# Kernel optimization log

Measured on AMD Instinct MI355X. Metric: run time of the kernel, lower is better.

## Reference

```python
import jax, jax.numpy as jnp
import numpy as np

B, CIN, COUT, T, S = 4, 32, 64, 8, 3   # batch, in-ch, out-ch, num_taps, stencil edge
D, H, W = 32, 64, 64                    # input volume
PAD = 1                                 # zero padding (stride 1) -> same spatial output


def setup_inputs() -> dict:
    key = jax.random.key(0)
    k1, k2, k3, k4 = jax.random.split(key, 4)
    x = jax.random.normal(k1, (B, CIN, D, H, W), jnp.float32)
    stencils = jax.random.normal(k2, (B, T, S, S, S), jnp.float32)
    weight = jax.random.normal(k3, (COUT, CIN, T), jnp.float32) * 0.05
    bias = jax.random.normal(k4, (COUT,), jnp.float32) * 0.05
    return {"x": x, "stencils": stencils, "weight": weight, "bias": bias}


def reference(x, stencils, weight, bias):
    # x: (B,Cin,D,H,W); stencils: (B,T,sx,sy,sz); weight: (Cout,Cin,T); bias: (Cout,)
    b, cin = x.shape[:2]
    t = stencils.shape[1]
    sx, sy, sz = stencils.shape[2:]
    # zero-pad spatially
    xp = jnp.pad(x, ((0, 0), (0, 0), (PAD, PAD), (PAD, PAD), (PAD, PAD)))
    # fold batch into channels -> grouped conv with groups = B*Cin (per-sample stencils)
    x_exp = xp.reshape(1, b * cin, xp.shape[2], xp.shape[3], xp.shape[4])
    # per-sample stencils shared across Cin, one output feature per (b, cin, tap)
    w = jnp.broadcast_to(stencils[:, None], (b, cin, t, sx, sy, sz))
    w = w.reshape(b * cin * t, 1, sx, sy, sz)
    tap = jax.lax.conv_general_dilated(
        x_exp, w,
        window_strides=(1, 1, 1), padding='VALID',
        dimension_numbers=('NCDHW', 'OIDHW', 'NCDHW'),
        feature_group_count=b * cin,
    )  # (1, B*Cin*T, Do, Ho, Wo)
    do, ho, wo = tap.shape[-3:]
    tap = tap.reshape(b, cin, t, do, ho, wo)
    # channel/tap mixing: (B,Cin,T,D,H,W) x (Cout,Cin,T) -> (B,Cout,D,H,W)
    y = jnp.einsum('bctdhw,oct->bodhw', tap, weight)
    return y + bias[None, :, None, None, None]
```

## Files before the change

kernel.cpp:

```cpp
#include <hip/hip_runtime.h>

typedef short bf16x8 __attribute__((ext_vector_type(8)));
typedef float f32x16 __attribute__((ext_vector_type(16)));

typedef const __attribute__((address_space(1))) unsigned int GUint;
typedef __attribute__((address_space(3))) unsigned int LUint;

#define XT_BYTES 37914624ull

__device__ __forceinline__ unsigned short f2bf(float f) {
    unsigned u = __float_as_uint(f);
    return (unsigned short)((u + 0x7FFFu + ((u >> 16) & 1u)) >> 16);
}

__global__ __launch_bounds__(256) void prep_x(const float* __restrict__ x,
                                              uint4* __restrict__ xt) {
    int yp = blockIdx.x;
    int zp = blockIdx.y;
    int b  = blockIdx.z;
    int t  = threadIdx.x;
    size_t rowbase = ((((size_t)b * 34 + zp) * 66 + yp) * 66) * 4;
    bool in_zy = (zp >= 1 && zp <= 32 && yp >= 1 && yp <= 64);
    for (int idx = t; idx < 264; idx += 256) {
        int q, xp;
        if (idx < 256) { q = idx >> 6; xp = idx & 63; }
        else { int k = idx - 256; q = k >> 1; xp = 64 + (k & 1); }
        uint4 v = make_uint4(0u, 0u, 0u, 0u);
        if (in_zy && xp >= 1 && xp <= 64) {
            int d = zp - 1, h = yp - 1, w = xp - 1;
            const float* xb = x + ((((size_t)b * 32 + q * 8) * 32 + d) * 64 + h) * 64 + w;
            unsigned short us[8];
            #pragma unroll
            for (int j = 0; j < 8; ++j)
                us[j] = f2bf(xb[(size_t)j * 131072]);
            v.x = us[0] | ((unsigned)us[1] << 16);
            v.y = us[2] | ((unsigned)us[3] << 16);
            v.z = us[4] | ((unsigned)us[5] << 16);
            v.w = us[6] | ((unsigned)us[7] << 16);
        }
        int pos = q ^ ((xp >> 1) & 3);
        xt[rowbase + (size_t)xp * 4 + pos] = v;
    }
}

__global__ __launch_bounds__(256) void prep_keff(const float* __restrict__ stencils,
                                                 const float* __restrict__ weight,
                                                 uint4* __restrict__ keffg) {
    int i = blockIdx.x * 256 + threadIdx.x;
    if (i >= 4 * 27 * 64 * 4) return;
    int q = i & 3;
    int o = (i >> 2) & 63;
    int br = i >> 8;
    int r = br % 27, b = br / 27;
    float st[8];
    #pragma unroll
    for (int t = 0; t < 8; ++t) st[t] = stencils[((size_t)b * 8 + t) * 27 + r];
    unsigned short us[8];
    #pragma unroll
    for (int j = 0; j < 8; ++j) {
        const float* wp = weight + ((size_t)o * 32 + q * 8 + j) * 8;
        float acc = 0.f;
        #pragma unroll
        for (int t = 0; t < 8; ++t) acc += wp[t] * st[t];
        us[j] = f2bf(acc);
    }
    uint4 v;
    v.x = us[0] | ((unsigned)us[1] << 16);
    v.y = us[2] | ((unsigned)us[3] << 16);
    v.z = us[4] | ((unsigned)us[5] << 16);
    v.w = us[6] | ((unsigned)us[7] << 16);
    int pos = q ^ ((o >> 1) & 3);
    keffg[(((size_t)br * 64 + o) << 2) + pos] = v;
}

#define KBUF 52224

__global__ __launch_bounds__(256, 2) void conv_mfma(
    const uint4* __restrict__ xt, const uint4* __restrict__ keffg,
    const float* __restrict__ bias, float* __restrict__ out) {
    __shared__ __align__(1024) char smem[60416];

    int n = blockIdx.x;
    int xcd = n & 7, local = n >> 3;
    int dt = local & 15;
    int cmb = (local >> 4) | (xcd << 4);
    int ht = cmb & 15, wt = (cmb >> 4) & 1, b = cmb >> 5;

    int tid = threadIdx.x;
    int lane = tid & 63, wid = tid >> 6;
    int nlo = lane & 31, kh = lane >> 5;

    const char* xtc = (const char*)xt;
    const char* kfc = (const char*)keffg;

    for (int row = wid; row < 24; row += 4) {
        int z = row / 6, yy = row - z * 6;
        size_t gbase = ((((size_t)b * 34 + dt * 2 + z) * 66 + ht * 4 + yy) * 66 + wt * 32) * 64;
        int ldsbase = row * 2176;
        #pragma unroll
        for (int cb = 0; cb < 136; cb += 64) {
            int rem = 136 - cb;
            if (lane < rem) {
                __builtin_amdgcn_global_load_lds(
                    (GUint*)(xtc + gbase + (size_t)(cb + lane) * 16),
                    (LUint*)(smem + ldsbase + cb * 16), 16, 0, 0);
            }
        }
    }
    __builtin_amdgcn_global_load_lds(
        (GUint*)(kfc + (size_t)(b * 27) * 4096 + (size_t)(wid * 64 + lane) * 16),
        (LUint*)(smem + KBUF + wid * 1024), 16, 0, 0);
    __syncthreads();

    int z = wid >> 1;
    int ys = (wid & 1) << 1;

    int Badr[2][3];
    #pragma unroll
    for (int s = 0; s < 2; ++s)
        #pragma unroll
        for (int k3 = 0; k3 < 3; ++k3) {
            int xl = nlo + k3;
            int pos = (s * 2 + kh) ^ ((xl >> 1) & 3);
            Badr[s][k3] = (z * 6 + ys) * 2176 + xl * 64 + (pos << 4);
        }
    int Aadr[2];
    #pragma unroll
    for (int s = 0; s < 2; ++s)
        Aadr[s] = nlo * 64 + (((s * 2 + kh) ^ ((nlo >> 1) & 3)) << 4);

    f32x16 acc[2][2];
    #pragma unroll
    for (int mt = 0; mt < 2; ++mt)
        #pragma unroll
        for (int nt = 0; nt < 2; ++nt)
            #pragma unroll
            for (int e = 0; e < 16; ++e) acc[mt][nt][e] = 0.f;

    #pragma unroll
    for (int r = 0; r < 27; ++r) {
        int i3 = r / 9, j3 = (r / 3) % 3, k3 = r % 3;
        if (r < 26) {
            __builtin_amdgcn_global_load_lds(
                (GUint*)(kfc + (size_t)(b * 27 + r + 1) * 4096 + (size_t)(wid * 64 + lane) * 16),
                (LUint*)(smem + KBUF + (((r + 1) & 1) << 12) + wid * 1024), 16, 0, 0);
        }
        int kbase = KBUF + ((r & 1) << 12);
        #pragma unroll
        for (int s = 0; s < 2; ++s) {
            bf16x8 a0 = *(const bf16x8*)(smem + kbase + Aadr[s]);
            bf16x8 a1 = *(const bf16x8*)(smem + kbase + 2048 + Aadr[s]);
            #pragma unroll
            for (int nt = 0; nt < 2; ++nt) {
                bf16x8 bb = *(const bf16x8*)(smem + (i3 * 6 + j3 + nt) * 2176 + Badr[s][k3]);
                acc[0][nt] = __builtin_amdgcn_mfma_f32_32x32x16_bf16(a0, bb, acc[0][nt], 0, 0, 0);
                acc[1][nt] = __builtin_amdgcn_mfma_f32_32x32x16_bf16(a1, bb, acc[1][nt], 0, 0, 0);
            }
        }
        __syncthreads();
    }

    int d = dt * 2 + z, w = wt * 32 + nlo;
    #pragma unroll
    for (int mt = 0; mt < 2; ++mt) {
        #pragma unroll
        for (int nt = 0; nt < 2; ++nt) {
            int h = ht * 4 + ys + nt;
            size_t sp = (((size_t)d) * 64 + h) * 64 + w;
            #pragma unroll
            for (int reg = 0; reg < 16; ++reg) {
                int o = mt * 32 + (reg & 3) + 8 * (reg >> 2) + 4 * kh;
                out[(((size_t)(b * 64 + o)) << 17) + sp] = acc[mt][nt][reg] + bias[o];
            }
        }
    }
}

extern "C" void kernel_launch(void* const* d_in, const int* in_sizes, int n_in,
                              void* d_out, int out_size, void* d_ws, size_t ws_size,
                              hipStream_t stream) {
    const float* x        = (const float*)d_in[0];
    const float* stencils = (const float*)d_in[1];
    const float* weight   = (const float*)d_in[2];
    const float* bias     = (const float*)d_in[3];
    float* out = (float*)d_out;

    uint4* xtbuf = (uint4*)d_ws;
    uint4* keffg = (uint4*)((char*)d_ws + XT_BYTES);

    prep_x<<<dim3(66, 34, 4), 256, 0, stream>>>(x, xtbuf);
    prep_keff<<<108, 256, 0, stream>>>(stencils, weight, keffg);
    conv_mfma<<<2048, 256, 0, stream>>>(xtbuf, keffg, bias, out);
}
```

Measured before the change: 257.9 us.

## Load effective kernel fragments directly into registers, drop per-tap LDS barriers

The effective-kernel tensor is pre-packed in MFMA A-fragment order, so each lane loads its fragments straight from global memory into registers with a one-tap-ahead prefetch. This removes the LDS staging buffer for the kernel and the __syncthreads after each of the 27 taps, which shrinks LDS usage and cuts barrier stalls. In exchange every wave fetches the same A fragments from global/L2 instead of sharing them through LDS, and register pressure rises from double-buffered fragments. The prep_x write order was also changed to a more contiguous per-thread pattern.

```diff
diff --git a/kernel.cpp b/kernel.cpp
--- a/kernel.cpp
+++ b/kernel.cpp
@@ -7,6 +7,7 @@
 typedef __attribute__((address_space(3))) unsigned int LUint;
 
 #define XT_BYTES 37914624ull
+#define XROW 2176
 
 __device__ __forceinline__ unsigned short f2bf(float f) {
     unsigned u = __float_as_uint(f);
@@ -22,9 +23,7 @@
     size_t rowbase = ((((size_t)b * 34 + zp) * 66 + yp) * 66) * 4;
     bool in_zy = (zp >= 1 && zp <= 32 && yp >= 1 && yp <= 64);
     for (int idx = t; idx < 264; idx += 256) {
-        int q, xp;
-        if (idx < 256) { q = idx >> 6; xp = idx & 63; }
-        else { int k = idx - 256; q = k >> 1; xp = 64 + (k & 1); }
+        int q = idx & 3, xp = idx >> 2;
         uint4 v = make_uint4(0u, 0u, 0u, 0u);
         if (in_zy && xp >= 1 && xp <= 64) {
             int d = zp - 1, h = yp - 1, w = xp - 1;
@@ -45,20 +44,23 @@
 
 __global__ __launch_bounds__(256) void prep_keff(const float* __restrict__ stencils,
                                                  const float* __restrict__ weight,
-                                                 uint4* __restrict__ keffg) {
+                                                 uint4* __restrict__ kf2) {
     int i = blockIdx.x * 256 + threadIdx.x;
-    if (i >= 4 * 27 * 64 * 4) return;
-    int q = i & 3;
-    int o = (i >> 2) & 63;
+    if (i >= 27648) return;
+    int lane = i & 63;
+    int mt = (i >> 6) & 1;
+    int s  = (i >> 7) & 1;
     int br = i >> 8;
     int r = br % 27, b = br / 27;
+    int o  = (lane & 31) + 32 * mt;
+    int cb = s * 16 + (lane >> 5) * 8;
     float st[8];
     #pragma unroll
     for (int t = 0; t < 8; ++t) st[t] = stencils[((size_t)b * 8 + t) * 27 + r];
     unsigned short us[8];
     #pragma unroll
     for (int j = 0; j < 8; ++j) {
-        const float* wp = weight + ((size_t)o * 32 + q * 8 + j) * 8;
+        const float* wp = weight + ((size_t)o * 32 + cb + j) * 8;
         float acc = 0.f;
         #pragma unroll
         for (int t = 0; t < 8; ++t) acc += wp[t] * st[t];
@@ -69,16 +71,13 @@
     v.y = us[2] | ((unsigned)us[3] << 16);
     v.z = us[4] | ((unsigned)us[5] << 16);
     v.w = us[6] | ((unsigned)us[7] << 16);
-    int pos = q ^ ((o >> 1) & 3);
-    keffg[(((size_t)br * 64 + o) << 2) + pos] = v;
+    kf2[i] = v;
 }
 
-#define KBUF 52224
-
 __global__ __launch_bounds__(256, 2) void conv_mfma(
-    const uint4* __restrict__ xt, const uint4* __restrict__ keffg,
+    const uint4* __restrict__ xt, const uint4* __restrict__ kf2,
     const float* __restrict__ bias, float* __restrict__ out) {
-    __shared__ __align__(1024) char smem[60416];
+    __shared__ __align__(1024) char smem[52224];
 
     int n = blockIdx.x;
     int xcd = n & 7, local = n >> 3;
@@ -91,12 +90,11 @@
     int nlo = lane & 31, kh = lane >> 5;
 
     const char* xtc = (const char*)xt;
-    const char* kfc = (const char*)keffg;
 
     for (int row = wid; row < 24; row += 4) {
         int z = row / 6, yy = row - z * 6;
         size_t gbase = ((((size_t)b * 34 + dt * 2 + z) * 66 + ht * 4 + yy) * 66 + wt * 32) * 64;
-        int ldsbase = row * 2176;
+        int ldsbase = row * XROW;
         #pragma unroll
         for (int cb = 0; cb < 136; cb += 64) {
             int rem = 136 - cb;
@@ -107,10 +105,6 @@
             }
         }
     }
-    __builtin_amdgcn_global_load_lds(
-        (GUint*)(kfc + (size_t)(b * 27) * 4096 + (size_t)(wid * 64 + lane) * 16),
-        (LUint*)(smem + KBUF + wid * 1024), 16, 0, 0);
-    __syncthreads();
 
     int z = wid >> 1;
     int ys = (wid & 1) << 1;
@@ -122,12 +116,15 @@
         for (int k3 = 0; k3 < 3; ++k3) {
             int xl = nlo + k3;
             int pos = (s * 2 + kh) ^ ((xl >> 1) & 3);
-            Badr[s][k3] = (z * 6 + ys) * 2176 + xl * 64 + (pos << 4);
+            Badr[s][k3] = (z * 6 + ys) * XROW + xl * 64 + (pos << 4);
         }
-    int Aadr[2];
+
+    const uint4* kfb = kf2 + (size_t)b * 27 * 256 + lane;
+
+    bf16x8 aCur[4], aNxt[4];
     #pragma unroll
-    for (int s = 0; s < 2; ++s)
-        Aadr[s] = nlo * 64 + (((s * 2 + kh) ^ ((nlo >> 1) & 3)) << 4);
+    for (int fi = 0; fi < 4; ++fi)
+        aCur[fi] = *(const bf16x8*)(kfb + fi * 64);
 
     f32x16 acc[2][2];
     #pragma unroll
@@ -137,27 +134,29 @@
             #pragma unroll
             for (int e = 0; e < 16; ++e) acc[mt][nt][e] = 0.f;
 
+    __syncthreads();
+
     #pragma unroll
     for (int r = 0; r < 27; ++r) {
-        int i3 = r / 9, j3 = (r / 3) % 3, k3 = r % 3;
+        const int i3 = r / 9, j3 = (r / 3) % 3, k3 = r % 3;
         if (r < 26) {
-            __builtin_amdgcn_global_load_lds(
-                (GUint*)(kfc + (size_t)(b * 27 + r + 1) * 4096 + (size_t)(wid * 64 + lane) * 16),
-                (LUint*)(smem + KBUF + (((r + 1) & 1) << 12) + wid * 1024), 16, 0, 0);
+            #pragma unroll
+            for (int fi = 0; fi < 4; ++fi)
+                aNxt[fi] = *(const bf16x8*)(kfb + ((r + 1) * 4 + fi) * 64);
         }
-        int kbase = KBUF + ((r & 1) << 12);
         #pragma unroll
         for (int s = 0; s < 2; ++s) {
-            bf16x8 a0 = *(const bf16x8*)(smem + kbase + Aadr[s]);
-            bf16x8 a1 = *(const bf16x8*)(smem + kbase + 2048 + Aadr[s]);
             #pragma unroll
             for (int nt = 0; nt < 2; ++nt) {
-                bf16x8 bb = *(const bf16x8*)(smem + (i3 * 6 + j3 + nt) * 2176 + Badr[s][k3]);
-                acc[0][nt] = __builtin_amdgcn_mfma_f32_32x32x16_bf16(a0, bb, acc[0][nt], 0, 0, 0);
-                acc[1][nt] = __builtin_amdgcn_mfma_f32_32x32x16_bf16(a1, bb, acc[1][nt], 0, 0, 0);
+                bf16x8 bb = *(const bf16x8*)(smem + (i3 * 6 + j3 + nt) * XROW + Badr[s][k3]);
+                acc[0][nt] = __builtin_amdgcn_mfma_f32_32x32x16_bf16(aCur[s * 2 + 0], bb, acc[0][nt], 0, 0, 0);
+                acc[1][nt] = __builtin_amdgcn_mfma_f32_32x32x16_bf16(aCur[s * 2 + 1], bb, acc[1][nt], 0, 0, 0);
             }
         }
-        __syncthreads();
+        if (r < 26) {
+            #pragma unroll
+            for (int fi = 0; fi < 4; ++fi) aCur[fi] = aNxt[fi];
+        }
     }
 
     int d = dt * 2 + z, w = wt * 32 + nlo;
@@ -186,9 +185,9 @@
     float* out = (float*)d_out;
 
     uint4* xtbuf = (uint4*)d_ws;
-    uint4* keffg = (uint4*)((char*)d_ws + XT_BYTES);
+    uint4* kf2   = (uint4*)((char*)d_ws + XT_BYTES);
 
     prep_x<<<dim3(66, 34, 4), 256, 0, stream>>>(x, xtbuf);
-    prep_keff<<<108, 256, 0, stream>>>(stencils, weight, keffg);
-    conv_mfma<<<2048, 256, 0, stream>>>(xtbuf, keffg, bias, out);
+    prep_keff<<<108, 256, 0, stream>>>(stencils, weight, kf2);
+    conv_mfma<<<2048, 256, 0, stream>>>(xtbuf, kf2, bias, out);
 }
```

After: 252.8 us. 1.02x faster.
